# Performance work log

Measured on AMD Instinct MI355X. Metric: run time of the kernel, lower is better.

Reference implementation:

```python
import jax, jax.numpy as jnp
import numpy as np

INPUT_SIZE = 4
HIDDEN_SIZE = 64
OUTPUT_SIZE = 40
BATCH = 4096
SEQ_LEN = 512


def setup_inputs() -> dict:
    key = jax.random.key(0)
    ks = jax.random.split(key, 7)
    s_ih = 1.0 / np.sqrt(HIDDEN_SIZE)
    x = jax.random.normal(ks[0], (BATCH, SEQ_LEN, INPUT_SIZE), dtype=jnp.float32)
    # PyTorch nn.RNN params, uniform(-1/sqrt(H), 1/sqrt(H))
    W_ih = jax.random.uniform(ks[1], (HIDDEN_SIZE, INPUT_SIZE), minval=-s_ih, maxval=s_ih, dtype=jnp.float32)
    W_hh = jax.random.uniform(ks[2], (HIDDEN_SIZE, HIDDEN_SIZE), minval=-s_ih, maxval=s_ih, dtype=jnp.float32)
    b_ih = jax.random.uniform(ks[3], (HIDDEN_SIZE,), minval=-s_ih, maxval=s_ih, dtype=jnp.float32)
    b_hh = jax.random.uniform(ks[4], (HIDDEN_SIZE,), minval=-s_ih, maxval=s_ih, dtype=jnp.float32)
    fc_W = jax.random.uniform(ks[5], (OUTPUT_SIZE, HIDDEN_SIZE), minval=-s_ih, maxval=s_ih, dtype=jnp.float32)
    fc_b = jax.random.uniform(ks[6], (OUTPUT_SIZE,), minval=-s_ih, maxval=s_ih, dtype=jnp.float32)
    return {"x": x, "W_ih": W_ih, "W_hh": W_hh, "b_ih": b_ih, "b_hh": b_hh, "fc_W": fc_W, "fc_b": fc_b}


def reference(x, W_ih, W_hh, b_ih, b_hh, fc_W, fc_b):
    B = x.shape[0]
    # Precompute input projections for all timesteps: [T, B, H]
    xp = jnp.einsum('bti,hi->tbh', x, W_ih) + (b_ih + b_hh)

    def step(h, xp_t):
        h = jnp.tanh(xp_t + h @ W_hh.T)
        return h, None

    h0 = jnp.zeros((B, HIDDEN_SIZE), dtype=x.dtype)
    h_last, _ = jax.lax.scan(step, h0, xp)
    # fc on last timestep hidden state
    return h_last @ fc_W.T + fc_b
```

## Files before the change

### kernel.cpp

```cpp
#include <hip/hip_runtime.h>
#include <math.h>

#define BATCH 4096
#define SEQ_T 512
#define ISZ   4
#define HID   64
#define OSZ   40
#define RPB   16

typedef __attribute__((ext_vector_type(8))) _Float16     half8;
typedef __attribute__((ext_vector_type(2))) _Float16     half2v;
typedef __attribute__((ext_vector_type(4))) float        float4v;
typedef __attribute__((ext_vector_type(2))) unsigned int uint2v;

static __device__ __forceinline__ half2v pk_f16(float a, float b) {
    return __builtin_bit_cast(half2v, __builtin_amdgcn_cvt_pkrtz(a, b));
}

static __device__ __forceinline__ float fast_tanh(float x) {
    float e = __builtin_amdgcn_exp2f(x * 2.885390081777927f);
    return fmaf(-2.0f, __builtin_amdgcn_rcpf(e + 1.0f), 1.0f);
}

#define LDS_BARRIER() asm volatile("s_waitcnt lgkmcnt(0)\n\ts_barrier" ::: "memory")

__global__ __launch_bounds__(512, 1)
void rnn_f16x2_kernel(const float* __restrict__ x,
                      const float* __restrict__ W_ih,
                      const float* __restrict__ W_hh,
                      const float* __restrict__ b_ih,
                      const float* __restrict__ b_hh,
                      const float* __restrict__ fc_W,
                      const float* __restrict__ fc_b,
                      float* __restrict__ out)
{
    __shared__ __attribute__((aligned(16))) _Float16 hterm[2][2][8][16][8];
    __shared__ __attribute__((aligned(16))) float hf[16][68];

    const int tid  = threadIdx.x;
    const int grp  = tid >> 8;
    const int wg   = (tid >> 6) & 3;
    const int lane = tid & 63;
    const int n    = lane & 15;
    const int q    = lane >> 4;
    const int blk0 = blockIdx.x * RPB;

    {
        unsigned int* p = (unsigned int*)hterm;
        #pragma unroll
        for (int i = tid; i < (int)(sizeof(hterm) / 4); i += 512) p[i] = 0u;
    }

    half8 A10, A11, A20, A21;
    {
        const float* wr = W_hh + (16 * wg + n) * HID;
        #pragma unroll
        for (int j = 0; j < 8; ++j) {
            float f0 = wr[     8 * q + j];
            float f1 = wr[32 + 8 * q + j];
            _Float16 h0 = (_Float16)f0; A10[j] = h0; A20[j] = (_Float16)(f0 - (float)h0);
            _Float16 h1 = (_Float16)f1; A11[j] = h1; A21[j] = (_Float16)(f1 - (float)h1);
        }
    }

    const int r0 = 16 * wg + 4 * q;
    float wih[4][4], bias[4];
    #pragma unroll
    for (int r = 0; r < 4; ++r) {
        bias[r] = b_ih[r0 + r] + b_hh[r0 + r];
        #pragma unroll
        for (int i = 0; i < ISZ; ++i) wih[r][i] = W_ih[(r0 + r) * ISZ + i];
    }

    const float* xrow = x + (size_t)(blk0 + n) * SEQ_T * ISZ;
    float4v x1 = *(const float4v*)(xrow + (size_t)(grp    ) * ISZ);
    float4v x2 = *(const float4v*)(xrow + (size_t)(grp + 2) * ISZ);
    float4v x3 = *(const float4v*)(xrow + (size_t)(grp + 4) * ISZ);
    int tnext = grp + 6;

    const int gw = 2 * wg + (q >> 1);
    const int j0 = 4 * (q & 1);

    float p0, p1, p2, p3;
    float hl0 = 0.f, hl1 = 0.f, hl2 = 0.f, hl3 = 0.f;

    __syncthreads();

#define MFMA16(A, B, C) __builtin_amdgcn_mfma_f32_16x16x32_f16((A), (B), (C), 0, 0, 0)

#define XP_COMPUTE()                                                           \
    {                                                                          \
        p0 = bias[0]; p1 = bias[1]; p2 = bias[2]; p3 = bias[3];                \
        _Pragma("unroll")                                                      \
        for (int i = 0; i < ISZ; ++i) {                                        \
            p0 = fmaf(x1[i], wih[0][i], p0);                                   \
            p1 = fmaf(x1[i], wih[1][i], p1);                                   \
            p2 = fmaf(x1[i], wih[2][i], p2);                                   \
            p3 = fmaf(x1[i], wih[3][i], p3);                                   \
        }                                                                      \
    }

#define XSHIFT()                                                               \
    {                                                                          \
        int tn = tnext; if (tn > SEQ_T - 1) tn = SEQ_T - 1;                    \
        float4v xf = *(const float4v*)(xrow + (size_t)tn * ISZ);               \
        tnext += 2;                                                            \
        x1 = x2; x2 = x3; x3 = xf;                                             \
    }

#define ACTIVE_STEP(RB, WB)                                                    \
    {                                                                          \
        half8 B10 = *(const half8*)&hterm[RB][0][    q][n][0];                 \
        half8 B11 = *(const half8*)&hterm[RB][0][4 + q][n][0];                 \
        half8 B20 = *(const half8*)&hterm[RB][1][    q][n][0];                 \
        half8 B21 = *(const half8*)&hterm[RB][1][4 + q][n][0];                 \
        float4v accA = {p0, p1, p2, p3};                                       \
        float4v accB = {0.f, 0.f, 0.f, 0.f};                                   \
        accA = MFMA16(A10, B10, accA);  accB = MFMA16(A11, B11, accB);         \
        accA = MFMA16(A10, B20, accA);  accB = MFMA16(A11, B21, accB);         \
        accA = MFMA16(A20, B10, accA);  accB = MFMA16(A21, B11, accB);         \
        hl0 = fast_tanh(accA[0] + accB[0]); hl1 = fast_tanh(accA[1] + accB[1]);\
        hl2 = fast_tanh(accA[2] + accB[2]); hl3 = fast_tanh(accA[3] + accB[3]);\
        half2v hi01 = pk_f16(hl0, hl1), hi23 = pk_f16(hl2, hl3);               \
        float s0 = hl0 - (float)hi01[0], s1 = hl1 - (float)hi01[1];            \
        float s2 = hl2 - (float)hi23[0], s3 = hl3 - (float)hi23[1];            \
        half2v lo01 = pk_f16(s0, s1), lo23 = pk_f16(s2, s3);                   \
        uint2v whi = { __builtin_bit_cast(unsigned int, hi01),                 \
                       __builtin_bit_cast(unsigned int, hi23) };               \
        uint2v wlo = { __builtin_bit_cast(unsigned int, lo01),                 \
                       __builtin_bit_cast(unsigned int, lo23) };               \
        *(uint2v*)&hterm[WB][0][gw][n][j0] = whi;                              \
        *(uint2v*)&hterm[WB][1][gw][n][j0] = wlo;                              \
    }

    if (grp == 0) {
        XP_COMPUTE(); XSHIFT();
        for (int it = 0; it < SEQ_T / 2; ++it) {
            ACTIVE_STEP(0, 1);
            LDS_BARRIER();
            XP_COMPUTE(); XSHIFT();
            LDS_BARRIER();
        }
    } else {
        for (int it = 0; it < SEQ_T / 2; ++it) {
            XP_COMPUTE(); XSHIFT();
            LDS_BARRIER();
            ACTIVE_STEP(1, 0);
            LDS_BARRIER();
        }
    }
#undef ACTIVE_STEP
#undef XSHIFT
#undef XP_COMPUTE
#undef MFMA16

    if (grp == 1) {
        float4v hv = {hl0, hl1, hl2, hl3};
        *(float4v*)&hf[n][r0] = hv;
    }
    __syncthreads();
    for (int it = tid; it < RPB * OSZ; it += 512) {
        const int b = it / OSZ;
        const int o = it - b * OSZ;
        const float* wo = fc_W + o * HID;
        float acc = fc_b[o];
        #pragma unroll
        for (int j = 0; j < HID; ++j)
            acc = fmaf(hf[b][j], wo[j], acc);
        out[(size_t)(blk0 + b) * OSZ + o] = acc;
    }
}

extern "C" void kernel_launch(void* const* d_in, const int* in_sizes, int n_in,
                              void* d_out, int out_size, void* d_ws, size_t ws_size,
                              hipStream_t stream) {
    const float* x    = (const float*)d_in[0];
    const float* W_ih = (const float*)d_in[1];
    const float* W_hh = (const float*)d_in[2];
    const float* b_ih = (const float*)d_in[3];
    const float* b_hh = (const float*)d_in[4];
    const float* fc_W = (const float*)d_in[5];
    const float* fc_b = (const float*)d_in[6];
    float* out = (float*)d_out;

    rnn_f16x2_kernel<<<BATCH / RPB, 512, 0, stream>>>(
        x, W_ih, W_hh, b_ih, b_hh, fc_W, fc_b, out);
}
```

Measured before the change: 216.5 us.

## Use rational tanh, independent MFMA chains, and raise wave priority in step

```diff
diff --git a/kernel.cpp b/kernel.cpp
--- a/kernel.cpp
+++ b/kernel.cpp
@@ -18,8 +18,21 @@
 }
 
 static __device__ __forceinline__ float fast_tanh(float x) {
-    float e = __builtin_amdgcn_exp2f(x * 2.885390081777927f);
-    return fmaf(-2.0f, __builtin_amdgcn_rcpf(e + 1.0f), 1.0f);
+    const float c = 7.90531110763549805f;
+    x = fminf(fmaxf(x, -c), c);
+    float t  = x * x;
+    float t2 = t * t;
+    float hi  = fmaf(t, -2.76076847742355e-16f, 2.00018790482477e-13f);
+    hi        = fmaf(t, hi, -8.60467152213735e-11f);
+    float mid = fmaf(t, 5.12229709037114e-08f, 1.48572235717979e-05f);
+    float lo  = fmaf(t, 6.37261928875436e-04f, 4.89352455891786e-03f);
+    float np  = fmaf(t2, hi, mid);
+    np        = fmaf(t2, np, lo);
+    float num = x * np;
+    float dp  = fmaf(t, 1.19825839466702e-06f, 1.18534705686654e-04f);
+    dp        = fmaf(t, dp, 2.26843463243900e-03f);
+    dp        = fmaf(t, dp, 4.89352518554385e-03f);
+    return num * __builtin_amdgcn_rcpf(dp);
 }
 
 #define LDS_BARRIER() asm volatile("s_waitcnt lgkmcnt(0)\n\ts_barrier" ::: "memory")
@@ -110,17 +123,23 @@
 
 #define ACTIVE_STEP(RB, WB)                                                    \
     {                                                                          \
+        __builtin_amdgcn_s_setprio(1);                                         \
         half8 B10 = *(const half8*)&hterm[RB][0][    q][n][0];                 \
         half8 B11 = *(const half8*)&hterm[RB][0][4 + q][n][0];                 \
         half8 B20 = *(const half8*)&hterm[RB][1][    q][n][0];                 \
         half8 B21 = *(const half8*)&hterm[RB][1][4 + q][n][0];                 \
-        float4v accA = {p0, p1, p2, p3};                                       \
-        float4v accB = {0.f, 0.f, 0.f, 0.f};                                   \
-        accA = MFMA16(A10, B10, accA);  accB = MFMA16(A11, B11, accB);         \
-        accA = MFMA16(A10, B20, accA);  accB = MFMA16(A11, B21, accB);         \
-        accA = MFMA16(A20, B10, accA);  accB = MFMA16(A21, B11, accB);         \
-        hl0 = fast_tanh(accA[0] + accB[0]); hl1 = fast_tanh(accA[1] + accB[1]);\
-        hl2 = fast_tanh(accA[2] + accB[2]); hl3 = fast_tanh(accA[3] + accB[3]);\
+        const float4v zz = {0.f, 0.f, 0.f, 0.f};                               \
+        float4v c1 = {p0, p1, p2, p3};                                         \
+        float4v a1 = MFMA16(A10, B10, c1);                                     \
+        float4v a2 = MFMA16(A11, B11, zz);                                     \
+        float4v a3 = MFMA16(A10, B20, zz);                                     \
+        float4v a4 = MFMA16(A11, B21, zz);                                     \
+        float4v a5 = MFMA16(A20, B10, zz);                                     \
+        float4v a6 = MFMA16(A21, B11, zz);                                     \
+        float4v s12 = a1 + a2, s34 = a3 + a4, s56 = a5 + a6;                   \
+        float4v sal = (s12 + s34) + s56;                                       \
+        hl0 = fast_tanh(sal[0]); hl1 = fast_tanh(sal[1]);                      \
+        hl2 = fast_tanh(sal[2]); hl3 = fast_tanh(sal[3]);                      \
         half2v hi01 = pk_f16(hl0, hl1), hi23 = pk_f16(hl2, hl3);               \
         float s0 = hl0 - (float)hi01[0], s1 = hl1 - (float)hi01[1];            \
         float s2 = hl2 - (float)hi23[0], s3 = hl3 - (float)hi23[1];            \
@@ -131,6 +150,7 @@
                        __builtin_bit_cast(unsigned int, lo23) };               \
         *(uint2v*)&hterm[WB][0][gw][n][j0] = whi;                              \
         *(uint2v*)&hterm[WB][1][gw][n][j0] = wlo;                              \
+        __builtin_amdgcn_s_setprio(0);                                         \
     }
 
     if (grp == 0) {
```

After: 250.9 us. 15.9% more time.
